# Kernel tuning notes

Hardware: AMD Instinct MI355X
Metric: run time of the kernel (lower is better)

The kernel has to match this reference:

```python
import jax, jax.numpy as jnp
import numpy as np


def setup_inputs() -> dict:
    key = jax.random.key(0)
    ks = jax.random.split(key, 7)
    B, I, H = 16384, 1024, 1024
    s = 1.0 / np.sqrt(H)
    return {
        "x": jax.random.normal(ks[0], (B, I), jnp.float32),
        "h_prev": jax.random.normal(ks[1], (B, H), jnp.float32),
        "c_prev": jax.random.normal(ks[2], (B, H), jnp.float32),
        "Wx": jax.random.normal(ks[3], (4, H, I), jnp.float32) * s,  # gates z,i,f,o
        "bx": jax.random.normal(ks[4], (4, H), jnp.float32) * s,
        "Rh": jax.random.normal(ks[5], (4, H, H), jnp.float32) * s,
        "bh": jax.random.normal(ks[6], (4, H), jnp.float32) * s,
    }


def reference(x, h_prev, c_prev, Wx, bx, Rh, bh):
    # Fused: 2 batched GEMMs for all 4 gates, then one elementwise block.
    # gates_x[g] = x @ Wx[g].T + bx[g]  (g in z,i,f,o), same for Rh/h_prev.
    gx = jnp.einsum('bi,ghi->gbh', x, Wx) + bx[:, None, :]       # [4,B,H]
    gh = jnp.einsum('bh,gkh->gbk', h_prev, Rh) + bh[:, None, :]  # [4,B,H]
    pre = gx + gh
    z = jnp.tanh(pre[0])
    i = jax.nn.sigmoid(pre[1])
    f = jax.nn.sigmoid(pre[2])
    o = jax.nn.sigmoid(pre[3])
    c = f * c_prev + i * z
    h = o * jnp.tanh(c)
    return (h, c)
```

## Files before the change

### kernel.cpp

```cpp
#include <hip/hip_runtime.h>
#include <stdint.h>

typedef __bf16 bf16;
typedef __bf16 bf16x4 __attribute__((ext_vector_type(4)));
typedef __bf16 bf16x8 __attribute__((ext_vector_type(8)));
typedef float  f32x4  __attribute__((ext_vector_type(4)));
typedef float  fvec4  __attribute__((ext_vector_type(4)));

#define B_DIM 16384
#define H_DIM 1024
#define K_DIM 2048
#define NKT   32

__device__ __forceinline__ void g2l16(const void* g, void* l) {
    __builtin_amdgcn_global_load_lds(
        (const __attribute__((address_space(1))) void*)g,
        (__attribute__((address_space(3))) void*)l,
        16, 0, 0);
}

__device__ __forceinline__ float sigm_fast(float x) {
    x = fminf(fmaxf(x, -40.f), 40.f);
    float e = __builtin_amdgcn_exp2f(-1.4426950408889634f * x);
    return __builtin_amdgcn_rcpf(1.0f + e);
}
__device__ __forceinline__ float tanh_fast(float x) {
    x = fminf(fmaxf(x, -40.f), 40.f);
    float e = __builtin_amdgcn_exp2f(-2.8853900817779268f * x);
    return (1.0f - e) * __builtin_amdgcn_rcpf(1.0f + e);
}

__global__ __launch_bounds__(256) void cvt_all(const float* __restrict__ x,
                                               const float* __restrict__ h,
                                               const float* __restrict__ Wx,
                                               const float* __restrict__ Rh,
                                               const float* __restrict__ bx,
                                               const float* __restrict__ bh,
                                               bf16* __restrict__ U,
                                               bf16* __restrict__ W,
                                               float* __restrict__ bb) {
    const int b   = blockIdx.x;
    const int tid = threadIdx.x;
    const float* src;
    bf16* dst;
    int half, blk;
    if (b < 8192) {
        src  = (b < 4096) ? x : h;
        half = (b < 4096) ? 0 : 1024;
        dst  = U;
        blk  = b & 4095;
    } else {
        int wb = b - 8192;
        src  = (wb < 1024) ? Wx : Rh;
        half = (wb < 1024) ? 0 : 1024;
        dst  = W;
        blk  = wb & 1023;
    }
    const float* s0 = src + (((size_t)blk << 2) << 10) + (tid << 2);
    bf16*        d0 = dst + (((size_t)blk << 2) << 11) + half + (tid << 2);
#pragma unroll
    for (int u = 0; u < 4; ++u) {
        fvec4 v = *(const fvec4*)(s0 + (u << 10));
        bf16x4 o = {(bf16)v.x, (bf16)v.y, (bf16)v.z, (bf16)v.w};
        *(bf16x4*)(d0 + (u << 11)) = o;
    }
    if (b == 0) {
        for (int i = tid; i < 4096; i += 256) bb[i] = bx[i] + bh[i];
    }
}

__global__ __launch_bounds__(512, 2)
void lstm_fused(const bf16* __restrict__ U, const bf16* __restrict__ W,
                const float* __restrict__ bb, const float* __restrict__ cprev,
                float* __restrict__ out) {
    __shared__ __align__(16) bf16 As[2][256 * 64];
    __shared__ __align__(16) bf16 Bs[2][256 * 64];

    const int tid  = threadIdx.x;
    const int wave = tid >> 6;
    const int lane = tid & 63;
    const int quad = lane >> 4;
    const int lc   = lane & 15;
    const int wm   = wave >> 2;
    const int wn   = wave & 3;

    int bid   = blockIdx.x;
    int xcd   = bid & 7;
    int t     = bid >> 3;
    int h_idx = (xcd << 1) + (t >> 6);
    int m_idx = t & 63;
    const int m0 = m_idx << 8;
    const int h0 = h_idx << 6;

    uint32_t offA[2][2], offB[2][2];
    uint32_t lofs[2];
#pragma unroll
    for (int ld = 0; ld < 2; ++ld) {
        int slot  = (ld << 9) + tid;
        int row   = slot >> 3;
        int chunk = slot & 7;
        int colb  = (chunk ^ (row & 7)) << 4;
        lofs[ld]  = slot << 4;
#pragma unroll
        for (int hf = 0; hf < 2; ++hf) {
            int arow = m0 + (hf << 7) + row;
            offA[ld][hf] = ((uint32_t)arow << 12) + colb;
            int br   = (hf << 7) + row;
            int gate = (br >> 4) & 3;
            int hl   = ((br >> 6) << 4) + (br & 15);
            int wrow = (gate << 10) + h0 + hl;
            offB[ld][hf] = ((uint32_t)wrow << 12) + colb;
        }
    }
    const char* Ub = (const char*)U;
    const char* Wb = (const char*)W;
    char* AsB = (char*)As;
    char* BsB = (char*)Bs;

#define STG_A(hf, dbuf, ktt) do {                                              \
        g2l16(Ub + offA[0][hf] + ((ktt) << 7),                                 \
              AsB + ((dbuf) << 15) + ((hf) << 14) + lofs[0]);                  \
        g2l16(Ub + offA[1][hf] + ((ktt) << 7),                                 \
              AsB + ((dbuf) << 15) + ((hf) << 14) + lofs[1]);                  \
    } while (0)
#define STG_B(hf, dbuf, ktt) do {                                              \
        g2l16(Wb + offB[0][hf] + ((ktt) << 7),                                 \
              BsB + ((dbuf) << 15) + ((hf) << 14) + lofs[0]);                  \
        g2l16(Wb + offB[1][hf] + ((ktt) << 7),                                 \
              BsB + ((dbuf) << 15) + ((hf) << 14) + lofs[1]);                  \
    } while (0)

#define LDFRAG(BASEB, dbuf, row, ks)                                           \
    (*(const bf16x8*)((BASEB) + ((dbuf) << 15) + ((row) << 7) +                \
                      ((((((ks) << 2)) + quad) ^ (lc & 7)) << 4)))

#define MFMA_Q(MIBASE, NIBASE)                                                 \
    do {                                                                       \
        _Pragma("unroll")                                                      \
        for (int mi = 0; mi < 4; ++mi)                                         \
            _Pragma("unroll")                                                  \
            for (int ni = 0; ni < 2; ++ni)                                     \
                _Pragma("unroll")                                              \
                for (int ks = 0; ks < 2; ++ks)                                 \
                    acc[(MIBASE) + mi][(NIBASE) + ni] =                        \
                        __builtin_amdgcn_mfma_f32_16x16x32_bf16(               \
                            a_[mi][ks], b_[(NIBASE) + ni][ks],                 \
                            acc[(MIBASE) + mi][(NIBASE) + ni], 0, 0, 0);       \
    } while (0)

    f32x4 acc[8][4];
#pragma unroll
    for (int mi = 0; mi < 8; ++mi)
#pragma unroll
        for (int ni = 0; ni < 4; ++ni)
            acc[mi][ni] = (f32x4){0.f, 0.f, 0.f, 0.f};

    STG_B(0, 0, 0);
    STG_A(0, 0, 0);
    STG_A(1, 0, 0);
    STG_B(1, 0, 0);
    STG_B(0, 1, 1);
    STG_A(0, 1, 1);
    asm volatile("s_waitcnt vmcnt(4)" ::: "memory");

    const int rA0 = (wm << 7) + lc;
    const int rB0 = (wn << 6) + lc;

    bf16x8 a_[4][2];
    bf16x8 b_[4][2];

#pragma clang loop unroll(disable)
    for (int kt = 0; kt < NKT; ++kt) {
        const int buf = kt & 1;

        __builtin_amdgcn_s_barrier();
        if (kt < NKT - 1) STG_A(1, buf ^ 1, kt + 1);
#pragma unroll
        for (int mi = 0; mi < 4; ++mi) {
            a_[mi][0] = LDFRAG(AsB, buf, rA0 + (mi << 4), 0);
            a_[mi][1] = LDFRAG(AsB, buf, rA0 + (mi << 4), 1);
        }
#pragma unroll
        for (int ni = 0; ni < 4; ++ni) {
            b_[ni][0] = LDFRAG(BsB, buf, rB0 + (ni << 4), 0);
            b_[ni][1] = LDFRAG(BsB, buf, rB0 + (ni << 4), 1);
        }
        __builtin_amdgcn_s_setprio(1);
        MFMA_Q(0, 0);
        __builtin_amdgcn_s_setprio(0);

        __builtin_amdgcn_s_barrier();
        if (kt < NKT - 1) STG_B(1, buf ^ 1, kt + 1);
        __builtin_amdgcn_s_setprio(1);
        MFMA_Q(0, 2);
        __builtin_amdgcn_s_setprio(0);
#pragma unroll
        for (int mi = 0; mi < 4; ++mi) {
            a_[mi][0] = LDFRAG(AsB, buf, rA0 + 64 + (mi << 4), 0);
            a_[mi][1] = LDFRAG(AsB, buf, rA0 + 64 + (mi << 4), 1);
        }

        __builtin_amdgcn_s_barrier();
        if (kt < NKT - 2) STG_B(0, buf, kt + 2);
        __builtin_amdgcn_s_setprio(1);
        MFMA_Q(4, 0);
        __builtin_amdgcn_s_setprio(0);

        __builtin_amdgcn_s_barrier();
        if (kt < NKT - 2) STG_A(0, buf, kt + 2);
        __builtin_amdgcn_s_setprio(1);
        MFMA_Q(4, 2);
        __builtin_amdgcn_s_setprio(0);
        if (kt < NKT - 2) {
            asm volatile("s_waitcnt vmcnt(4)" ::: "memory");
        } else if (kt == NKT - 2) {
            asm volatile("s_waitcnt vmcnt(0)" ::: "memory");
        }
    }

    const int h = h0 + (wn << 4) + lc;
    float bias[4];
#pragma unroll
    for (int g = 0; g < 4; ++g) bias[g] = bb[(g << 10) + h];

    float* out_h = out;
    float* out_c = out + (size_t)B_DIM * H_DIM;
#pragma unroll
    for (int mi = 0; mi < 8; ++mi) {
#pragma unroll
        for (int r = 0; r < 4; ++r) {
            int brow  = m0 + (wm << 7) + (mi << 4) + (quad << 2) + r;
            size_t rb = (size_t)brow << 10;
            float zp = acc[mi][0][r] + bias[0];
            float ip = acc[mi][1][r] + bias[1];
            float fp = acc[mi][2][r] + bias[2];
            float op = acc[mi][3][r] + bias[3];
            float zz = tanh_fast(zp);
            float ii = sigm_fast(ip);
            float ff = sigm_fast(fp);
            float oo = sigm_fast(op);
            float cp = cprev[rb + h];
            float cn = ff * cp + ii * zz;
            float hn = oo * tanh_fast(cn);
            out_h[rb + h] = hn;
            out_c[rb + h] = cn;
        }
    }
}

extern "C" void kernel_launch(void* const* d_in, const int* in_sizes, int n_in,
                              void* d_out, int out_size, void* d_ws, size_t ws_size,
                              hipStream_t stream) {
    const float* x  = (const float*)d_in[0];
    const float* hp = (const float*)d_in[1];
    const float* cp = (const float*)d_in[2];
    const float* Wx = (const float*)d_in[3];
    const float* bx = (const float*)d_in[4];
    const float* Rh = (const float*)d_in[5];
    const float* bh = (const float*)d_in[6];

    bf16*  U  = (bf16*)d_ws;
    bf16*  W  = (bf16*)((char*)d_ws + (size_t)67108864);
    float* bb = (float*)((char*)d_ws + (size_t)67108864 + 16777216);

    cvt_all<<<10240, 256, 0, stream>>>(x, hp, Wx, Rh, bx, bh, U, W, bb);
    lstm_fused<<<1024, 512, 0, stream>>>(U, W, bb, cp, (float*)d_out);
}
```

Baseline: 550.7 us.

## Use 4-wave blocks with 128x128 per-wave tiles and simplified double buffering

Halves threads per block to four waves, each computing a 128x128 output tile with 64 accumulator fragments, and gives each thread more of the global-to-LDS staging loads. Replaces the interleaved four-barrier schedule with setprio by a single issue-wait-barrier-compute double-buffered loop. The aim is higher register-level data reuse per fragment load and fewer barriers. The cost is far higher register pressure, lower wave occupancy per CU and less overlap of loads with MFMA work.

```diff
diff --git a/kernel.cpp b/kernel.cpp
--- a/kernel.cpp
+++ b/kernel.cpp
@@ -69,7 +69,7 @@
     }
 }
 
-__global__ __launch_bounds__(512, 2)
+__global__ __launch_bounds__(256, 1)
 void lstm_fused(const bf16* __restrict__ U, const bf16* __restrict__ W,
                 const float* __restrict__ bb, const float* __restrict__ cprev,
                 float* __restrict__ out) {
@@ -81,8 +81,8 @@
     const int lane = tid & 63;
     const int quad = lane >> 4;
     const int lc   = lane & 15;
-    const int wm   = wave >> 2;
-    const int wn   = wave & 3;
+    const int wm   = wave >> 1;
+    const int wn   = wave & 1;
 
     int bid   = blockIdx.x;
     int xcd   = bid & 7;
@@ -92,11 +92,11 @@
     const int m0 = m_idx << 8;
     const int h0 = h_idx << 6;
 
-    uint32_t offA[2][2], offB[2][2];
-    uint32_t lofs[2];
-#pragma unroll
-    for (int ld = 0; ld < 2; ++ld) {
-        int slot  = (ld << 9) + tid;
+    uint32_t offA[4][2], offB[4][2];
+    uint32_t lofs[4];
+#pragma unroll
+    for (int ld = 0; ld < 4; ++ld) {
+        int slot  = (ld << 8) + tid;
         int row   = slot >> 3;
         int chunk = slot & 7;
         int colb  = (chunk ^ (row & 7)) << 4;
@@ -117,111 +117,75 @@
     char* AsB = (char*)As;
     char* BsB = (char*)Bs;
 
-#define STG_A(hf, dbuf, ktt) do {                                              \
-        g2l16(Ub + offA[0][hf] + ((ktt) << 7),                                 \
-              AsB + ((dbuf) << 15) + ((hf) << 14) + lofs[0]);                  \
-        g2l16(Ub + offA[1][hf] + ((ktt) << 7),                                 \
-              AsB + ((dbuf) << 15) + ((hf) << 14) + lofs[1]);                  \
-    } while (0)
-#define STG_B(hf, dbuf, ktt) do {                                              \
-        g2l16(Wb + offB[0][hf] + ((ktt) << 7),                                 \
-              BsB + ((dbuf) << 15) + ((hf) << 14) + lofs[0]);                  \
-        g2l16(Wb + offB[1][hf] + ((ktt) << 7),                                 \
-              BsB + ((dbuf) << 15) + ((hf) << 14) + lofs[1]);                  \
+#define STG_ALL(dbuf, ktt) do {                                                \
+        _Pragma("unroll")                                                      \
+        for (int hf = 0; hf < 2; ++hf)                                         \
+            _Pragma("unroll")                                                  \
+            for (int ld = 0; ld < 4; ++ld)                                     \
+                g2l16(Ub + offA[ld][hf] + ((ktt) << 7),                        \
+                      AsB + ((dbuf) << 15) + (hf << 14) + lofs[ld]);           \
+        _Pragma("unroll")                                                      \
+        for (int hf = 0; hf < 2; ++hf)                                         \
+            _Pragma("unroll")                                                  \
+            for (int ld = 0; ld < 4; ++ld)                                     \
+                g2l16(Wb + offB[ld][hf] + ((ktt) << 7),                        \
+                      BsB + ((dbuf) << 15) + (hf << 14) + lofs[ld]);           \
     } while (0)
 
 #define LDFRAG(BASEB, dbuf, row, ks)                                           \
     (*(const bf16x8*)((BASEB) + ((dbuf) << 15) + ((row) << 7) +                \
                       ((((((ks) << 2)) + quad) ^ (lc & 7)) << 4)))
 
-#define MFMA_Q(MIBASE, NIBASE)                                                 \
-    do {                                                                       \
-        _Pragma("unroll")                                                      \
-        for (int mi = 0; mi < 4; ++mi)                                         \
-            _Pragma("unroll")                                                  \
-            for (int ni = 0; ni < 2; ++ni)                                     \
-                _Pragma("unroll")                                              \
-                for (int ks = 0; ks < 2; ++ks)                                 \
-                    acc[(MIBASE) + mi][(NIBASE) + ni] =                        \
-                        __builtin_amdgcn_mfma_f32_16x16x32_bf16(               \
-                            a_[mi][ks], b_[(NIBASE) + ni][ks],                 \
-                            acc[(MIBASE) + mi][(NIBASE) + ni], 0, 0, 0);       \
-    } while (0)
-
-    f32x4 acc[8][4];
+    f32x4 acc[8][8];
 #pragma unroll
     for (int mi = 0; mi < 8; ++mi)
 #pragma unroll
-        for (int ni = 0; ni < 4; ++ni)
+        for (int ni = 0; ni < 8; ++ni)
             acc[mi][ni] = (f32x4){0.f, 0.f, 0.f, 0.f};
 
-    STG_B(0, 0, 0);
-    STG_A(0, 0, 0);
-    STG_A(1, 0, 0);
-    STG_B(1, 0, 0);
-    STG_B(0, 1, 1);
-    STG_A(0, 1, 1);
-    asm volatile("s_waitcnt vmcnt(4)" ::: "memory");
+    STG_ALL(0, 0);
 
     const int rA0 = (wm << 7) + lc;
-    const int rB0 = (wn << 6) + lc;
-
-    bf16x8 a_[4][2];
-    bf16x8 b_[4][2];
+    const int rB0 = (wn << 7) + lc;
 
 #pragma clang loop unroll(disable)
     for (int kt = 0; kt < NKT; ++kt) {
         const int buf = kt & 1;
 
         __builtin_amdgcn_s_barrier();
-        if (kt < NKT - 1) STG_A(1, buf ^ 1, kt + 1);
-#pragma unroll
-        for (int mi = 0; mi < 4; ++mi) {
-            a_[mi][0] = LDFRAG(AsB, buf, rA0 + (mi << 4), 0);
-            a_[mi][1] = LDFRAG(AsB, buf, rA0 + (mi << 4), 1);
-        }
-#pragma unroll
-        for (int ni = 0; ni < 4; ++ni) {
-            b_[ni][0] = LDFRAG(BsB, buf, rB0 + (ni << 4), 0);
-            b_[ni][1] = LDFRAG(BsB, buf, rB0 + (ni << 4), 1);
-        }
-        __builtin_amdgcn_s_setprio(1);
-        MFMA_Q(0, 0);
-        __builtin_amdgcn_s_setprio(0);
-
+        if (kt < NKT - 1) STG_ALL(buf ^ 1, kt + 1);
+        if (kt < NKT - 1) {
+            asm volatile("s_waitcnt vmcnt(16)" ::: "memory");
+        } else {
+            asm volatile("s_waitcnt vmcnt(0)" ::: "memory");
+        }
         __builtin_amdgcn_s_barrier();
-        if (kt < NKT - 1) STG_B(1, buf ^ 1, kt + 1);
-        __builtin_amdgcn_s_setprio(1);
-        MFMA_Q(0, 2);
-        __builtin_amdgcn_s_setprio(0);
-#pragma unroll
-        for (int mi = 0; mi < 4; ++mi) {
-            a_[mi][0] = LDFRAG(AsB, buf, rA0 + 64 + (mi << 4), 0);
-            a_[mi][1] = LDFRAG(AsB, buf, rA0 + 64 + (mi << 4), 1);
-        }
-
-        __builtin_amdgcn_s_barrier();
-        if (kt < NKT - 2) STG_B(0, buf, kt + 2);
-        __builtin_amdgcn_s_setprio(1);
-        MFMA_Q(4, 0);
-        __builtin_amdgcn_s_setprio(0);
-
-        __builtin_amdgcn_s_barrier();
-        if (kt < NKT - 2) STG_A(0, buf, kt + 2);
-        __builtin_amdgcn_s_setprio(1);
-        MFMA_Q(4, 2);
-        __builtin_amdgcn_s_setprio(0);
-        if (kt < NKT - 2) {
-            asm volatile("s_waitcnt vmcnt(4)" ::: "memory");
-        } else if (kt == NKT - 2) {
-            asm volatile("s_waitcnt vmcnt(0)" ::: "memory");
-        }
-    }
-
-    const int h = h0 + (wn << 4) + lc;
-    float bias[4];
-#pragma unroll
-    for (int g = 0; g < 4; ++g) bias[g] = bb[(g << 10) + h];
+
+#pragma unroll
+        for (int ks = 0; ks < 2; ++ks) {
+            bf16x8 a_[8], b_[8];
+#pragma unroll
+            for (int mi = 0; mi < 8; ++mi)
+                a_[mi] = LDFRAG(AsB, buf, rA0 + (mi << 4), ks);
+#pragma unroll
+            for (int ni = 0; ni < 8; ++ni)
+                b_[ni] = LDFRAG(BsB, buf, rB0 + (ni << 4), ks);
+#pragma unroll
+            for (int mi = 0; mi < 8; ++mi)
+#pragma unroll
+                for (int ni = 0; ni < 8; ++ni)
+                    acc[mi][ni] = __builtin_amdgcn_mfma_f32_16x16x32_bf16(
+                        a_[mi], b_[ni], acc[mi][ni], 0, 0, 0);
+        }
+    }
+
+    const int hb = h0 + (wn << 5) + lc;
+    float bias[2][4];
+#pragma unroll
+    for (int hg = 0; hg < 2; ++hg)
+#pragma unroll
+        for (int g = 0; g < 4; ++g)
+            bias[hg][g] = bb[(g << 10) + hb + (hg << 4)];
 
     float* out_h = out;
     float* out_c = out + (size_t)B_DIM * H_DIM;
@@ -231,19 +195,23 @@
         for (int r = 0; r < 4; ++r) {
             int brow  = m0 + (wm << 7) + (mi << 4) + (quad << 2) + r;
             size_t rb = (size_t)brow << 10;
-            float zp = acc[mi][0][r] + bias[0];
-            float ip = acc[mi][1][r] + bias[1];
-            float fp = acc[mi][2][r] + bias[2];
-            float op = acc[mi][3][r] + bias[3];
-            float zz = tanh_fast(zp);
-            float ii = sigm_fast(ip);
-            float ff = sigm_fast(fp);
-            float oo = sigm_fast(op);
-            float cp = cprev[rb + h];
-            float cn = ff * cp + ii * zz;
-            float hn = oo * tanh_fast(cn);
-            out_h[rb + h] = hn;
-            out_c[rb + h] = cn;
+#pragma unroll
+            for (int hg = 0; hg < 2; ++hg) {
+                const int h = hb + (hg << 4);
+                float zp = acc[mi][(hg << 2) + 0][r] + bias[hg][0];
+                float ip = acc[mi][(hg << 2) + 1][r] + bias[hg][1];
+                float fp = acc[mi][(hg << 2) + 2][r] + bias[hg][2];
+                float op = acc[mi][(hg << 2) + 3][r] + bias[hg][3];
+                float zz = tanh_fast(zp);
+                float ii = sigm_fast(ip);
+                float ff = sigm_fast(fp);
+                float oo = sigm_fast(op);
+                float cp = cprev[rb + h];
+                float cn = ff * cp + ii * zz;
+                float hn = oo * tanh_fast(cn);
+                out_h[rb + h] = hn;
+                out_c[rb + h] = cn;
+            }
         }
     }
 }
@@ -264,5 +232,5 @@
     float* bb = (float*)((char*)d_ws + (size_t)67108864 + 16777216);
 
     cvt_all<<<10240, 256, 0, stream>>>(x, hp, Wx, Rh, bx, bh, U, W, bb);
-    lstm_fused<<<1024, 512, 0, stream>>>(U, W, bb, cp, (float*)d_out);
-}
+    lstm_fused<<<1024, 256, 0, stream>>>(U, W, bb, cp, (float*)d_out);
+}
```

Result: slower. 1.153 ms (+109.5%).
